# Kernel optimization log

Hardware: AMD Instinct MI355X
Metric: run time of the kernel (lower is better)

Reference implementation:

```python
import jax, jax.numpy as jnp
import numpy as np

N_NODES = 100000


def gcn_conv(x, edge_index, W, b):
    # PyG GCNConv: add self-loops, symmetric normalization D^-1/2 (A+I) D^-1/2, then linear.
    n = x.shape[0]
    loop = jnp.arange(n, dtype=edge_index.dtype)
    src = jnp.concatenate([edge_index[0], loop])
    dst = jnp.concatenate([edge_index[1], loop])
    deg = jax.ops.segment_sum(jnp.ones_like(dst, dtype=x.dtype), dst, num_segments=n)
    dinv = jnp.where(deg > 0, jax.lax.rsqrt(deg), 0.0)
    norm = dinv[src] * dinv[dst]                      # [E+N]
    h = x @ W                                          # [N, out]
    msg = h[src] * norm[:, None]                       # gather + scale
    out = jax.ops.segment_sum(msg, dst, num_segments=n)  # scatter-add
    return out + b


def forward_one(x, edge_index, W1, b1, W2, b2, fc_w, fc_b):
    x = jax.nn.relu(gcn_conv(x, edge_index, W1, b1))
    x = jax.nn.relu(gcn_conv(x, edge_index, W2, b2))
    x = jnp.mean(x, axis=0)                            # [hidden]
    return x @ fc_w.T + fc_b


def setup_inputs() -> dict:
    key = jax.random.key(0)
    ks = jax.random.split(key, 10)
    d_in, d_h = 64, 64
    E = 1600000
    s = 1.0 / np.sqrt(d_in)
    return {
        "x1": jax.random.normal(ks[0], (N_NODES, d_in), jnp.float32),
        "x2": jax.random.normal(ks[1], (N_NODES, d_in), jnp.float32),
        "edge_index1": jax.random.randint(ks[2], (2, E), 0, N_NODES, jnp.int32),
        "edge_index2": jax.random.randint(ks[3], (2, E), 0, N_NODES, jnp.int32),
        "W1": jax.random.normal(ks[4], (d_in, d_h), jnp.float32) * s,
        "b1": jnp.zeros((d_h,), jnp.float32),
        "W2": jax.random.normal(ks[5], (d_h, d_h), jnp.float32) * s,
        "b2": jnp.zeros((d_h,), jnp.float32),
        "fc_w": jax.random.normal(ks[6], (d_h, d_h), jnp.float32) * s,
        "fc_b": jnp.zeros((d_h,), jnp.float32),
    }


def reference(x1, x2, edge_index1, edge_index2, W1, b1, W2, b2, fc_w, fc_b):
    out1 = forward_one(x1, edge_index1, W1, b1, W2, b2, fc_w, fc_b)
    out2 = forward_one(x2, edge_index2, W1, b1, W2, b2, fc_w, fc_b)
    return (out1, out2)
```

## Files before the change

kernel.cpp:

```cpp
#include <hip/hip_runtime.h>


#define TPB    256
#define CHUNK  128
#define SHIFT  7
#define KMAX   1024
#define CAP    2560
#define EPB    8192
#define CPAD   16

typedef __attribute__((ext_vector_type(8))) short short8;
typedef __attribute__((ext_vector_type(4))) float f32x4;
typedef __attribute__((ext_vector_type(2))) float float2v;
typedef __attribute__((ext_vector_type(2))) unsigned int uint2v;

struct Ctx {
    const float* X; const int* esrc; const int* edst;
    unsigned int* temp; unsigned char* Hs2; unsigned char* Hs;
    unsigned int* csr; int* row_ptr; int* degA; float* dinv; int* cursorG;
    float* P; float* P2; float* outp;
};

__device__ __forceinline__ unsigned short f2bf(float x) {
    union { float f; unsigned int i; } c; c.f = x;
    unsigned int r = c.i + 0x7FFFu + ((c.i >> 16) & 1u);
    return (unsigned short)(r >> 16);
}
__device__ __forceinline__ unsigned char f2fp8(float x) {
    int p = __builtin_amdgcn_cvt_pk_fp8_f32(x, x, 0, false);
    return (unsigned char)(p & 0xFF);
}
__device__ __forceinline__ float2v up8lo(unsigned int w) {
    return __builtin_amdgcn_cvt_pk_f32_fp8(w, false);
}
__device__ __forceinline__ float2v up8hi(unsigned int w) {
    return __builtin_amdgcn_cvt_pk_f32_fp8(w, true);
}

__global__ void k_prepW2(const float* __restrict__ W1, const float* __restrict__ W2,
                         unsigned short* __restrict__ Wt1, unsigned short* __restrict__ Wt2) {
    const float* W = blockIdx.x ? W2 : W1;
    unsigned short* Wt = blockIdx.x ? Wt2 : Wt1;
    for (int i = threadIdx.x; i < 64 * 64; i += 256) {
        int n = i >> 6, k = i & 63;
        Wt[i] = f2bf(W[k * 64 + n]);
    }
}

__global__ void k_zeroCur(Ctx c0, Ctx c1, int nb0, int K, int N) {
    int b = blockIdx.x; Ctx c = c0;
    if (b >= nb0) { c = c1; b -= nb0; }
    int i = b * blockDim.x + threadIdx.x;
    if (i < K) c.cursorG[i * CPAD] = 0;
    if (b == 0 && threadIdx.x < 64) c.Hs[(size_t)N * 64 + threadIdx.x] = 0;
}

__global__ __launch_bounds__(1024) void k_binA(Ctx c0, Ctx c1, int nb0, int E, int K) {
    __shared__ int cnt[KMAX];
    __shared__ int ofs[KMAX];
    __shared__ int segBase[KMAX];
    __shared__ int wsum[16];
    __shared__ unsigned int sorted[EPB];
    __shared__ unsigned short bkt[EPB];
    int b = blockIdx.x; Ctx c = c0;
    if (b >= nb0) { c = c1; b -= nb0; }
    int tid = threadIdx.x;
    cnt[tid] = 0;
    __syncthreads();
    int base = b * EPB;
    int tot = E - base; if (tot > EPB) tot = EPB;
#pragma unroll
    for (int k = 0; k < EPB / 1024; ++k) {
        int e = base + k * 1024 + tid;
        if (e < E) atomicAdd(&cnt[c.edst[e] >> SHIFT], 1);
    }
    __syncthreads();
    int v = cnt[tid];
    int lane = tid & 63, w = tid >> 6;
    int x = v;
#pragma unroll
    for (int off = 1; off < 64; off <<= 1) {
        int t = __shfl_up(x, off, 64);
        if (lane >= off) x += t;
    }
    if (lane == 63) wsum[w] = x;
    __syncthreads();
    if (tid < 16) {
        int y = wsum[tid];
#pragma unroll
        for (int off = 1; off < 16; off <<= 1) {
            int t = __shfl_up(y, off, 16);
            if ((tid & 15) >= off) y += t;
        }
        wsum[tid] = y;
    }
    __syncthreads();
    int pre = w ? wsum[w - 1] : 0;
    ofs[tid] = x + pre - v;
    if (tid < K) {
        segBase[tid] = v ? atomicAdd(&c.cursorG[tid * CPAD], v) : 0;
    } else {
        segBase[tid] = 0;
    }
    cnt[tid] = 0;
    __syncthreads();
#pragma unroll
    for (int k = 0; k < EPB / 1024; ++k) {
        int e = base + k * 1024 + tid;
        if (e < E) {
            int d = c.edst[e];
            int bk = d >> SHIFT;
            int r = atomicAdd(&cnt[bk], 1);
            int p = ofs[bk] + r;
            sorted[p] = ((unsigned int)(d & (CHUNK - 1)) << 17) | (unsigned int)c.esrc[e];
            bkt[p] = (unsigned short)bk;
        }
    }
    __syncthreads();
    for (int p = tid; p < tot; p += 1024) {
        unsigned int vv = sorted[p];
        int bk = bkt[p];
        int pos = segBase[bk] + (p - ofs[bk]);
        if (pos < CAP) c.temp[(size_t)bk * CAP + pos] = vv;
    }
}

__global__ __launch_bounds__(256) void k_csrb(Ctx c0, Ctx c1, int nb0, int N) {
    __shared__ int deg[CHUNK];
    __shared__ int lofs[CHUNK];
    __shared__ int cur[CHUNK];
    __shared__ int wsum2[2];
    int b = blockIdx.x; Ctx c = c0;
    if (b >= nb0) { c = c1; b -= nb0; }
    int tid = threadIdx.x;
    if (tid < CHUNK) deg[tid] = 0;
    __syncthreads();
    int cnt = c.cursorG[b * CPAD]; if (cnt > CAP) cnt = CAP;
    const size_t tb = (size_t)b * CAP;
    for (int i = tid; i < cnt; i += 256) atomicAdd(&deg[c.temp[tb + i] >> 17], 1);
    __syncthreads();
    int vdeg = 0, x = 0;
    if (tid < CHUNK) { vdeg = deg[tid]; x = vdeg; }
#pragma unroll
    for (int off = 1; off < 64; off <<= 1) {
        int t = __shfl_up(x, off, 64);
        if ((tid & 63) >= off) x += t;
    }
    if (tid < CHUNK && (tid & 63) == 63) wsum2[tid >> 6] = x;
    __syncthreads();
    int base = b * CAP;
    if (tid < CHUNK) {
        int pre = (tid >> 6) ? wsum2[0] : 0;
        int excl = x + pre - vdeg;
        lofs[tid] = excl;
        cur[tid] = 0;
        int node = b * CHUNK + tid;
        if (node < N) {
            c.row_ptr[node] = base + excl;
            c.degA[node] = vdeg;
            c.dinv[node] = rsqrtf((float)vdeg + 1.0f);
        }
    }
    __syncthreads();
    for (int i = tid; i < cnt; i += 256) {
        unsigned int p = c.temp[tb + i];
        int dl = p >> 17;
        int rank = atomicAdd(&cur[dl], 1);
        c.csr[base + lofs[dl] + rank] = (p & 0x1FFFFu) << 6;
    }
}

__device__ __forceinline__ void mfma_tail(short8 a0, short8 a1,
                                          const unsigned short* __restrict__ Wt,
                                          unsigned char* __restrict__ Hs,
                                          int row0, int r, int q, int N) {
    short8 bfrag[4][2];
#pragma unroll
    for (int ct = 0; ct < 4; ++ct)
#pragma unroll
        for (int kb = 0; kb < 2; ++kb)
            bfrag[ct][kb] = *(const short8*)(Wt + (ct * 16 + r) * 64 + q * 8 + 32 * kb);
    f32x4 acc[4];
#pragma unroll
    for (int ct = 0; ct < 4; ++ct) {
        acc[ct] = (f32x4){0.0f, 0.0f, 0.0f, 0.0f};
        acc[ct] = __builtin_amdgcn_mfma_f32_16x16x32_bf16(a0, bfrag[ct][0], acc[ct], 0, 0, 0);
        acc[ct] = __builtin_amdgcn_mfma_f32_16x16x32_bf16(a1, bfrag[ct][1], acc[ct], 0, 0, 0);
    }
#pragma unroll
    for (int reg = 0; reg < 4; ++reg) {
        int row = row0 + q * 4 + reg;
        if (row < N) {
            size_t base = (size_t)row * 64 + r;
#pragma unroll
            for (int ct = 0; ct < 4; ++ct)
                Hs[base + ct * 16] = f2fp8(acc[ct][reg]);
        }
    }
}

__global__ __launch_bounds__(256) void k_gemm1(Ctx c0, Ctx c1, int nb0,
                                               const unsigned short* __restrict__ Wt,
                                               int nTiles, int N) {
    int b = blockIdx.x; Ctx c = c0;
    if (b >= nb0) { c = c1; b -= nb0; }
    int wave = threadIdx.x >> 6, lane = threadIdx.x & 63;
    int tile = b * 4 + wave;
    if (tile >= nTiles) return;
    int r = lane & 15, q = lane >> 4;
    int row0 = tile * 16;
    int row = row0 + r;
    int rr = row < N ? row : N - 1;
    float d = c.dinv[rr];
    const float* xrow = c.X + (size_t)rr * 64 + q * 8;
    short8 a0, a1;
#pragma unroll
    for (int j = 0; j < 8; ++j) a0[j] = (short)f2bf(xrow[j] * d);
#pragma unroll
    for (int j = 0; j < 8; ++j) a1[j] = (short)f2bf(xrow[32 + j] * d);
    mfma_tail(a0, a1, Wt, c.Hs, row0, r, q, N);
}

__device__ __forceinline__ void agg_map(int bi, int nb0, int swz,
                                        const Ctx& c0, const Ctx& c1,
                                        Ctx& c, int& b) {
    if (swz) {
        int graph = (bi >> 2) & 1;
        b = ((bi >> 3) << 2) | (bi & 3);
        c = graph ? c1 : c0;
    } else {
        b = bi; c = c0;
        if (b >= nb0) { c = c1; b -= nb0; }
    }
}

__device__ __forceinline__ void agg_issue8w(const unsigned char* __restrict__ Hs,
                                            unsigned int idx, int lim,
                                            int hbase, int j, unsigned int s8,
                                            uint2v* h) {
#pragma unroll
    for (int u = 0; u < 8; ++u) {
        if (4 * u >= lim) break;
        unsigned int su = (unsigned int)__shfl((int)idx, hbase + 4 * u + j, 64);
        h[u] = *(const uint2v*)(Hs + (su | s8));
    }
}
__device__ __forceinline__ void agg_cons8w(const uint2v* h, int lim, float2v* acc) {
#pragma unroll
    for (int u = 0; u < 8; ++u) {
        if (4 * u >= lim) break;
        acc[0] += up8lo(h[u][0]); acc[1] += up8hi(h[u][0]);
        acc[2] += up8lo(h[u][1]); acc[3] += up8hi(h[u][1]);
    }
}

__device__ __forceinline__ void agg_pair2(const unsigned char* __restrict__ Hs,
                                          const unsigned int* __restrict__ csr,
                                          int beg0, int deg0, int maxs0,
                                          int beg1, int deg1, int maxs1,
                                          int lane, unsigned int sent,
                                          float2v* acc0, float2v* acc1) {
    int hbase = lane & 32;
    int hl = lane & 31;
    int j = (hl >> 3) & 3;
    unsigned int s8 = (unsigned int)((lane & 7) * 8);
    unsigned int idx0 = (hl < deg0) ? csr[beg0 + hl] : sent;
    unsigned int idx1 = (hl < deg1) ? csr[beg1 + hl] : sent;
    int lim0 = maxs0 > 32 ? 32 : maxs0;
    int lim1 = maxs1 > 32 ? 32 : maxs1;
    uint2v h0[8], h1[8];
    agg_issue8w(Hs, idx0, lim0, hbase, j, s8, h0);
    agg_issue8w(Hs, idx1, lim1, hbase, j, s8, h1);
    agg_cons8w(h0, lim0, acc0);
    agg_cons8w(h1, lim1, acc1);
    for (int base = 32; base < maxs0; base += 32) {
        unsigned int idx = (base + hl < deg0) ? csr[beg0 + base + hl] : sent;
        int lim = maxs0 - base; if (lim > 32) lim = 32;
        uint2v hh[8];
        agg_issue8w(Hs, idx, lim, hbase, j, s8, hh);
        agg_cons8w(hh, lim, acc0);
    }
    for (int base = 32; base < maxs1; base += 32) {
        unsigned int idx = (base + hl < deg1) ? csr[beg1 + base + hl] : sent;
        int lim = maxs1 - base; if (lim > 32) lim = 32;
        uint2v hh[8];
        agg_issue8w(Hs, idx, lim, hbase, j, s8, hh);
        agg_cons8w(hh, lim, acc1);
    }
#pragma unroll
    for (int k = 0; k < 4; ++k) {
        float2v o;
        o.x = __shfl_xor(acc0[k].x, 8, 64);  o.y = __shfl_xor(acc0[k].y, 8, 64);
        acc0[k] += o;
        o.x = __shfl_xor(acc0[k].x, 16, 64); o.y = __shfl_xor(acc0[k].y, 16, 64);
        acc0[k] += o;
        o.x = __shfl_xor(acc1[k].x, 8, 64);  o.y = __shfl_xor(acc1[k].y, 8, 64);
        acc1[k] += o;
        o.x = __shfl_xor(acc1[k].x, 16, 64); o.y = __shfl_xor(acc1[k].y, 16, 64);
        acc1[k] += o;
    }
}

__global__ __launch_bounds__(256, 8) void k_agg1(Ctx c0, Ctx c1, int nb0, int swz,
                                                 const float* __restrict__ bias,
                                                 const unsigned short* __restrict__ Wt2,
                                                 int n) {
    __shared__ unsigned short As[16][64];
    Ctx c; int b;
    agg_map(blockIdx.x, nb0, swz, c0, c1, c, b);
    int wave = threadIdx.x >> 6, lane = threadIdx.x & 63;
    int h = lane >> 5;
    int nbase = b * 16 + wave * 4;
    int node0 = nbase + h;
    int node1 = nbase + 2 + h;
    int nd0 = node0 < n ? node0 : 0;
    int nd1 = node1 < n ? node1 : 0;
    int beg0 = c.row_ptr[nd0];
    int beg1 = c.row_ptr[nd1];
    int deg0 = (node0 < n) ? c.degA[nd0] : 0;
    int deg1 = (node1 < n) ? c.degA[nd1] : 0;
    int od0 = __shfl_xor(deg0, 32, 64); int m0 = deg0 > od0 ? deg0 : od0;
    int od1 = __shfl_xor(deg1, 32, 64); int m1 = deg1 > od1 ? deg1 : od1;
    int maxs0 = __builtin_amdgcn_readfirstlane(m0);
    int maxs1 = __builtin_amdgcn_readfirstlane(m1);
    if (b == 0 && threadIdx.x < 64) c.Hs2[(size_t)n * 64 + threadIdx.x] = 0;
    float2v acc0[4] = {{0.f,0.f},{0.f,0.f},{0.f,0.f},{0.f,0.f}};
    float2v acc1[4] = {{0.f,0.f},{0.f,0.f},{0.f,0.f},{0.f,0.f}};
    agg_pair2(c.Hs, c.csr, beg0, deg0, maxs0, beg1, deg1, maxs1,
              lane, (unsigned int)n << 6, acc0, acc1);
    if (((lane >> 3) & 3) == 0) {
        int s = lane & 7;
#pragma unroll
        for (int pr = 0; pr < 2; ++pr) {
            const float2v* ac = pr ? acc1 : acc0;
            int node = nbase + pr * 2 + h;
            ushort4 oA = {0, 0, 0, 0}, oB = {0, 0, 0, 0};
            if (node < n) {
                uint2v hv = *(const uint2v*)(c.Hs + (size_t)node * 64 + s * 8);
                float2v h0 = up8lo(hv[0]), h1 = up8hi(hv[0]);
                float2v h2 = up8lo(hv[1]), h3 = up8hi(hv[1]);
                float4 ba = *(const float4*)(bias + s * 8);
                float4 bb = *(const float4*)(bias + s * 8 + 4);
                float d = c.dinv[node];
                oA.x = f2bf(fmaxf(ba.x + d * (ac[0].x + h0.x), 0.0f) * d);
                oA.y = f2bf(fmaxf(ba.y + d * (ac[0].y + h0.y), 0.0f) * d);
                oA.z = f2bf(fmaxf(ba.z + d * (ac[1].x + h1.x), 0.0f) * d);
                oA.w = f2bf(fmaxf(ba.w + d * (ac[1].y + h1.y), 0.0f) * d);
                oB.x = f2bf(fmaxf(bb.x + d * (ac[2].x + h2.x), 0.0f) * d);
                oB.y = f2bf(fmaxf(bb.y + d * (ac[2].y + h2.y), 0.0f) * d);
                oB.z = f2bf(fmaxf(bb.z + d * (ac[3].x + h3.x), 0.0f) * d);
                oB.w = f2bf(fmaxf(bb.w + d * (ac[3].y + h3.y), 0.0f) * d);
            }
            int row = wave * 4 + pr * 2 + h;
            int col = (s * 8) ^ ((row & 7) << 3);
            *(ushort4*)(&As[row][col]) = oA;
            *(ushort4*)(&As[row][col + 4]) = oB;
        }
    }
    __syncthreads();
    {
        int r = lane & 15, q = lane >> 4;
        int sw = (r & 7) << 3;
        short8 a0 = *(const short8*)(&As[r][(q * 8) ^ sw]);
        short8 a1 = *(const short8*)(&As[r][(q * 8 + 32) ^ sw]);
        const unsigned short* wp = Wt2 + (wave * 16 + r) * 64 + q * 8;
        short8 b0 = *(const short8*)(wp);
        short8 b1 = *(const short8*)(wp + 32);
        f32x4 acc2 = {0.0f, 0.0f, 0.0f, 0.0f};
        acc2 = __builtin_amdgcn_mfma_f32_16x16x32_bf16(a0, b0, acc2, 0, 0, 0);
        acc2 = __builtin_amdgcn_mfma_f32_16x16x32_bf16(a1, b1, acc2, 0, 0, 0);
#pragma unroll
        for (int reg = 0; reg < 4; ++reg) {
            int l = q * 4 + reg;
            int row = b * 16 + l;
            if (row < n)
                c.Hs2[(size_t)row * 64 + wave * 16 + r] = f2fp8(acc2[reg]);
        }
    }
}

__global__ __launch_bounds__(256, 8) void k_agg2(Ctx c0, Ctx c1, int nb0, int swz,
                                                 const float* __restrict__ bias, int n) {
    __shared__ float red[16 * 64];
    Ctx c; int b;
    agg_map(blockIdx.x, nb0, swz, c0, c1, c, b);
    int wave = threadIdx.x >> 6, lane = threadIdx.x & 63;
    int h = lane >> 5;
    int nbase = b * 16 + wave * 4;
    int node0 = nbase + h;
    int node1 = nbase + 2 + h;
    int nd0 = node0 < n ? node0 : 0;
    int nd1 = node1 < n ? node1 : 0;
    int beg0 = c.row_ptr[nd0];
    int beg1 = c.row_ptr[nd1];
    int deg0 = (node0 < n) ? c.degA[nd0] : 0;
    int deg1 = (node1 < n) ? c.degA[nd1] : 0;
    int od0 = __shfl_xor(deg0, 32, 64); int m0 = deg0 > od0 ? deg0 : od0;
    int od1 = __shfl_xor(deg1, 32, 64); int m1 = deg1 > od1 ? deg1 : od1;
    int maxs0 = __builtin_amdgcn_readfirstlane(m0);
    int maxs1 = __builtin_amdgcn_readfirstlane(m1);
    float2v acc0[4] = {{0.f,0.f},{0.f,0.f},{0.f,0.f},{0.f,0.f}};
    float2v acc1[4] = {{0.f,0.f},{0.f,0.f},{0.f,0.f},{0.f,0.f}};
    agg_pair2(c.Hs2, c.csr, beg0, deg0, maxs0, beg1, deg1, maxs1,
              lane, (unsigned int)n << 6, acc0, acc1);
    if (((lane >> 3) & 3) == 0) {
        int s = lane & 7;
#pragma unroll
        for (int pr = 0; pr < 2; ++pr) {
            const float2v* ac = pr ? acc1 : acc0;
            int node = nbase + pr * 2 + h;
            float4 vA = {0.f, 0.f, 0.f, 0.f}, vB = {0.f, 0.f, 0.f, 0.f};
            if (node < n) {
                uint2v hv = *(const uint2v*)(c.Hs2 + (size_t)node * 64 + s * 8);
                float2v h0 = up8lo(hv[0]), h1 = up8hi(hv[0]);
                float2v h2 = up8lo(hv[1]), h3 = up8hi(hv[1]);
                float4 ba = *(const float4*)(bias + s * 8);
                float4 bb = *(const float4*)(bias + s * 8 + 4);
                float d = c.dinv[node];
                vA.x = fmaxf(ba.x + d * (ac[0].x + h0.x), 0.0f);
                vA.y = fmaxf(ba.y + d * (ac[0].y + h0.y), 0.0f);
                vA.z = fmaxf(ba.z + d * (ac[1].x + h1.x), 0.0f);
                vA.w = fmaxf(ba.w + d * (ac[1].y + h1.y), 0.0f);
                vB.x = fmaxf(bb.x + d * (ac[2].x + h2.x), 0.0f);
                vB.y = fmaxf(bb.y + d * (ac[2].y + h2.y), 0.0f);
                vB.z = fmaxf(bb.z + d * (ac[3].x + h3.x), 0.0f);
                vB.w = fmaxf(bb.w + d * (ac[3].y + h3.y), 0.0f);
            }
            int row = wave * 4 + pr * 2 + h;
            *(float4*)(&red[row * 64 + s * 8]) = vA;
            *(float4*)(&red[row * 64 + s * 8 + 4]) = vB;
        }
    }
    __syncthreads();
    if (threadIdx.x < 64) {
        float acc16 = 0.0f;
#pragma unroll
        for (int r = 0; r < 16; ++r) acc16 += red[r * 64 + threadIdx.x];
        c.P[(size_t)b * 64 + threadIdx.x] = acc16;
    }
}

__global__ void k_colsum(Ctx c0, Ctx c1, int nb0, int rows) {
    int b = blockIdx.x; Ctx c = c0;
    if (b >= nb0) { c = c1; b -= nb0; }
    int f = threadIdx.x;
    float acc = 0.0f;
    for (int r = b; r < rows; r += nb0) acc += c.P[(size_t)r * 64 + f];
    c.P2[b * 64 + f] = acc;
}

__global__ void k_fc(Ctx c0, Ctx c1, const float* __restrict__ fcw,
                     const float* __restrict__ fcb, int n) {
    Ctx c = blockIdx.x ? c1 : c0;
    __shared__ float S[64];
    int j = threadIdx.x;
    float s = 0.0f;
    for (int r = 0; r < 256; ++r) s += c.P2[r * 64 + j];
    S[j] = s;
    __syncthreads();
    float inv = 1.0f / (float)n;
    float acc = fcb[j];
#pragma unroll
    for (int k = 0; k < 64; ++k) acc += (S[k] * inv) * fcw[j * 64 + k];
    c.outp[j] = acc;
}

extern "C" void kernel_launch(void* const* d_in, const int* in_sizes, int n_in,
                              void* d_out, int out_size, void* d_ws, size_t ws_size,
                              hipStream_t stream) {
    const float* x[2]  = {(const float*)d_in[0], (const float*)d_in[1]};
    const int*   ei[2] = {(const int*)d_in[2], (const int*)d_in[3]};
    const float* W1  = (const float*)d_in[4];
    const float* b1  = (const float*)d_in[5];
    const float* W2  = (const float*)d_in[6];
    const float* b2  = (const float*)d_in[7];
    const float* fcw = (const float*)d_in[8];
    const float* fcb = (const float*)d_in[9];
    float* out = (float*)d_out;

    const int N  = in_sizes[0] / 64;
    const int E  = in_sizes[2] / 2;
    const int NF = N * 64;
    const int K  = (N + CHUNK - 1) / CHUNK;
    const int gGm  = (N + 15) / 16;
    const int gGmP = (gGm + 3) & ~3;
    const int nTiles = (N + 15) / 16;
    const int gMf = (nTiles + 3) / 4;
    const int gBin = (E + EPB - 1) / EPB;
    const int gK  = (K + TPB - 1) / TPB;

    auto al = [](size_t x) { return (x + 127) & ~(size_t)127; };
    size_t tempB = (size_t)K * CAP * 4;
    size_t hs2B  = (size_t)NF + 64;
    size_t szRegion = al(tempB > hs2B ? tempB : hs2B);
    size_t szHs  = al((size_t)NF + 64);
    size_t szCsr = al((size_t)K * CAP * 4);
    size_t szRp  = al((size_t)N * 4);
    size_t szDeg = al((size_t)N * 4);
    size_t szDi  = al((size_t)N * 4);
    size_t szCu  = al((size_t)K * CPAD * 4);
    size_t szP   = al((size_t)gGmP * 64 * 4);
    size_t szP2  = al((size_t)256 * 64 * 4);
    size_t setB  = szRegion + szHs + szCsr + szRp + szDeg + szDi + szCu + szP + szP2;
    size_t wtB   = 2 * al(64 * 64 * 2);
    bool batched = ws_size >= wtB + 2 * setB;

    char* base = (char*)d_ws;
    unsigned short* Wt1 = (unsigned short*)base;
    unsigned short* Wt2 = (unsigned short*)(base + al(64 * 64 * 2));

    auto mkctx = [&](int g, char* p) {
        Ctx c;
        c.X = x[g]; c.esrc = ei[g]; c.edst = ei[g] + E;
        c.temp = (unsigned int*)p; c.Hs2 = (unsigned char*)p; p += szRegion;
        c.Hs = (unsigned char*)p; p += szHs;
        c.csr = (unsigned int*)p; p += szCsr;
        c.row_ptr = (int*)p; p += szRp;
        c.degA = (int*)p; p += szDeg;
        c.dinv = (float*)p; p += szDi;
        c.cursorG = (int*)p; p += szCu;
        c.P = (float*)p; p += szP;
        c.P2 = (float*)p;
        c.outp = out + g * 64;
        return c;
    };
    char* set0 = base + wtB;
    Ctx c0 = mkctx(0, set0);
    Ctx c1 = mkctx(1, batched ? set0 + setB : set0);

    k_prepW2<<<2, 256, 0, stream>>>(W1, W2, Wt1, Wt2);

    auto pipe = [&](Ctx A, Ctx B, int mult) {
        int swz = (mult == 2) ? 1 : 0;
        k_zeroCur<<<mult * gK, TPB, 0, stream>>>(A, B, gK, K, N);
        k_binA<<<mult * gBin, 1024, 0, stream>>>(A, B, gBin, E, K);
        k_csrb<<<mult * K, 256, 0, stream>>>(A, B, K, N);
        k_gemm1<<<mult * gMf, 256, 0, stream>>>(A, B, gMf, Wt1, nTiles, N);
        k_agg1<<<mult * gGmP, 256, 0, stream>>>(A, B, gGmP, swz, b1, Wt2, N);
        k_agg2<<<mult * gGmP, 256, 0, stream>>>(A, B, gGmP, swz, b2, N);
        k_colsum<<<mult * 256, 64, 0, stream>>>(A, B, 256, gGmP);
        k_fc<<<mult, 64, 0, stream>>>(A, B, fcw, fcb, N);
    };

    if (batched) {
        pipe(c0, c1, 2);
    } else {
        pipe(c0, c0, 1);
        pipe(c1, c1, 1);
    }
}
```

Measured before the change: 280.7 us.

## Sort nodes by in-degree so aggregation waves process similar-degree nodes

Builds a degree histogram during CSR construction and a new kernel that scatters node ids into a degree-bucketed permutation. The two aggregation kernels then pick nodes through this permutation, so the lanes of a wave handle nodes of similar degree and idle less in the max-degree loop. The cost is an extra kernel launch, global atomics, and scattered row accesses to Hs/Hs2, which lose the locality of consecutive node ids.

```diff
diff --git a/kernel.cpp b/kernel.cpp
--- a/kernel.cpp
+++ b/kernel.cpp
@@ -18,6 +18,7 @@
     const float* X; const int* esrc; const int* edst;
     unsigned int* temp; unsigned char* Hs2; unsigned char* Hs;
     unsigned int* csr; int* row_ptr; int* degA; float* dinv; int* cursorG;
+    int* perm; int* dcnt;
     float* P; float* P2; float* outp;
 };
 
@@ -52,6 +53,7 @@
     if (b >= nb0) { c = c1; b -= nb0; }
     int i = b * blockDim.x + threadIdx.x;
     if (i < K) c.cursorG[i * CPAD] = 0;
+    if (b == 0 && threadIdx.x < 128) c.dcnt[threadIdx.x] = 0;
     if (b == 0 && threadIdx.x < 64) c.Hs[(size_t)N * 64 + threadIdx.x] = 0;
 }
 
@@ -130,10 +132,12 @@
     __shared__ int lofs[CHUNK];
     __shared__ int cur[CHUNK];
     __shared__ int wsum2[2];
+    __shared__ int dh[64];
     int b = blockIdx.x; Ctx c = c0;
     if (b >= nb0) { c = c1; b -= nb0; }
     int tid = threadIdx.x;
     if (tid < CHUNK) deg[tid] = 0;
+    if (tid >= CHUNK && tid < CHUNK + 64) dh[tid - CHUNK] = 0;
     __syncthreads();
     int cnt = c.cursorG[b * CPAD]; if (cnt > CAP) cnt = CAP;
     const size_t tb = (size_t)b * CAP;
@@ -159,14 +163,40 @@
             c.row_ptr[node] = base + excl;
             c.degA[node] = vdeg;
             c.dinv[node] = rsqrtf((float)vdeg + 1.0f);
-        }
-    }
-    __syncthreads();
+            atomicAdd(&dh[vdeg < 63 ? vdeg : 63], 1);
+        }
+    }
+    __syncthreads();
+    if (tid < 64 && dh[tid]) atomicAdd(&c.dcnt[tid], dh[tid]);
     for (int i = tid; i < cnt; i += 256) {
         unsigned int p = c.temp[tb + i];
         int dl = p >> 17;
         int rank = atomicAdd(&cur[dl], 1);
         c.csr[base + lofs[dl] + rank] = (p & 0x1FFFFu) << 6;
+    }
+}
+
+__global__ __launch_bounds__(256) void k_dperm(Ctx c0, Ctx c1, int nb0, int N) {
+    __shared__ int dbase[64];
+    int b = blockIdx.x; Ctx c = c0;
+    if (b >= nb0) { c = c1; b -= nb0; }
+    if (threadIdx.x < 64) {
+        int v = c.dcnt[threadIdx.x];
+        int x = v;
+#pragma unroll
+        for (int off = 1; off < 64; off <<= 1) {
+            int t = __shfl_up(x, off, 64);
+            if (threadIdx.x >= off) x += t;
+        }
+        dbase[threadIdx.x] = x - v;
+    }
+    __syncthreads();
+    int node = b * 256 + threadIdx.x;
+    if (node < N) {
+        int dg = c.degA[node];
+        int dc = dg < 63 ? dg : 63;
+        int pos = dbase[dc] + atomicAdd(&c.dcnt[64 + dc], 1);
+        c.perm[pos] = node;
     }
 }
 
@@ -310,9 +340,11 @@
     agg_map(blockIdx.x, nb0, swz, c0, c1, c, b);
     int wave = threadIdx.x >> 6, lane = threadIdx.x & 63;
     int h = lane >> 5;
-    int nbase = b * 16 + wave * 4;
-    int node0 = nbase + h;
-    int node1 = nbase + 2 + h;
+    int pbase = b * 16 + wave * 4;
+    int pidx0 = pbase + h;
+    int pidx1 = pbase + 2 + h;
+    int node0 = pidx0 < n ? c.perm[pidx0] : n;
+    int node1 = pidx1 < n ? c.perm[pidx1] : n;
     int nd0 = node0 < n ? node0 : 0;
     int nd1 = node1 < n ? node1 : 0;
     int beg0 = c.row_ptr[nd0];
@@ -333,7 +365,7 @@
 #pragma unroll
         for (int pr = 0; pr < 2; ++pr) {
             const float2v* ac = pr ? acc1 : acc0;
-            int node = nbase + pr * 2 + h;
+            int node = pr ? node1 : node0;
             ushort4 oA = {0, 0, 0, 0}, oB = {0, 0, 0, 0};
             if (node < n) {
                 uint2v hv = *(const uint2v*)(c.Hs + (size_t)node * 64 + s * 8);
@@ -372,9 +404,11 @@
 #pragma unroll
         for (int reg = 0; reg < 4; ++reg) {
             int l = q * 4 + reg;
-            int row = b * 16 + l;
-            if (row < n)
+            int pidx = b * 16 + l;
+            if (pidx < n) {
+                int row = c.perm[pidx];
                 c.Hs2[(size_t)row * 64 + wave * 16 + r] = f2fp8(acc2[reg]);
+            }
         }
     }
 }
@@ -386,9 +420,11 @@
     agg_map(blockIdx.x, nb0, swz, c0, c1, c, b);
     int wave = threadIdx.x >> 6, lane = threadIdx.x & 63;
     int h = lane >> 5;
-    int nbase = b * 16 + wave * 4;
-    int node0 = nbase + h;
-    int node1 = nbase + 2 + h;
+    int pbase = b * 16 + wave * 4;
+    int pidx0 = pbase + h;
+    int pidx1 = pbase + 2 + h;
+    int node0 = pidx0 < n ? c.perm[pidx0] : n;
+    int node1 = pidx1 < n ? c.perm[pidx1] : n;
     int nd0 = node0 < n ? node0 : 0;
     int nd1 = node1 < n ? node1 : 0;
     int beg0 = c.row_ptr[nd0];
@@ -408,7 +444,7 @@
 #pragma unroll
         for (int pr = 0; pr < 2; ++pr) {
             const float2v* ac = pr ? acc1 : acc0;
-            int node = nbase + pr * 2 + h;
+            int node = pr ? node1 : node0;
             float4 vA = {0.f, 0.f, 0.f, 0.f}, vB = {0.f, 0.f, 0.f, 0.f};
             if (node < n) {
                 uint2v hv = *(const uint2v*)(c.Hs2 + (size_t)node * 64 + s * 8);
@@ -488,6 +524,7 @@
     const int gMf = (nTiles + 3) / 4;
     const int gBin = (E + EPB - 1) / EPB;
     const int gK  = (K + TPB - 1) / TPB;
+    const int gPm = (N + 255) / 256;
 
     auto al = [](size_t x) { return (x + 127) & ~(size_t)127; };
     size_t tempB = (size_t)K * CAP * 4;
@@ -499,9 +536,12 @@
     size_t szDeg = al((size_t)N * 4);
     size_t szDi  = al((size_t)N * 4);
     size_t szCu  = al((size_t)K * CPAD * 4);
+    size_t szPerm = al((size_t)N * 4);
+    size_t szDc  = al(128 * 4);
     size_t szP   = al((size_t)gGmP * 64 * 4);
     size_t szP2  = al((size_t)256 * 64 * 4);
-    size_t setB  = szRegion + szHs + szCsr + szRp + szDeg + szDi + szCu + szP + szP2;
+    size_t setB  = szRegion + szHs + szCsr + szRp + szDeg + szDi + szCu
+                 + szPerm + szDc + szP + szP2;
     size_t wtB   = 2 * al(64 * 64 * 2);
     bool batched = ws_size >= wtB + 2 * setB;
 
@@ -519,6 +559,8 @@
         c.degA = (int*)p; p += szDeg;
         c.dinv = (float*)p; p += szDi;
         c.cursorG = (int*)p; p += szCu;
+        c.perm = (int*)p; p += szPerm;
+        c.dcnt = (int*)p; p += szDc;
         c.P = (float*)p; p += szP;
         c.P2 = (float*)p;
         c.outp = out + g * 64;
@@ -535,6 +577,7 @@
         k_zeroCur<<<mult * gK, TPB, 0, stream>>>(A, B, gK, K, N);
         k_binA<<<mult * gBin, 1024, 0, stream>>>(A, B, gBin, E, K);
         k_csrb<<<mult * K, 256, 0, stream>>>(A, B, K, N);
+        k_dperm<<<mult * gPm, 256, 0, stream>>>(A, B, gPm, N);
         k_gemm1<<<mult * gMf, 256, 0, stream>>>(A, B, gMf, Wt1, nTiles, N);
         k_agg1<<<mult * gGmP, 256, 0, stream>>>(A, B, gGmP, swz, b1, Wt2, N);
         k_agg2<<<mult * gGmP, 256, 0, stream>>>(A, B, gGmP, swz, b2, N);
```

Result: slower. 667.3 us (+137.7%).
